# Performance work log

Hardware: AMD Instinct MI355X
Metric: run time of the kernel (lower is better)

The kernel has to match this reference:

```python
import jax, jax.numpy as jnp
import numpy as np

B, T, S_ENC, D = 2, 1024, 1024, 2048
NQ, NKV, H = 16, 8, 256
EPS = 1e-6
CAP = 50.0
SCALE = 0.0625  # query_pre_attn_scalar = head_dim**-0.5
BASE = 10000
K_MASK = -2.3819763e+38


def rms_norm(x, scale, eps=EPS):
    var = jnp.mean(jnp.square(x), axis=-1, keepdims=True)
    return x * jax.lax.rsqrt(var + eps) * (1.0 + scale)


def apply_rope(x, positions, base=BASE):
    # x: [B, L, N, H], positions: [B, L] float. rope_proportion=1.0 -> full head.
    head_dim = x.shape[-1]
    timescale = base ** (2.0 / head_dim * jnp.arange(head_dim // 2, dtype=jnp.float32))
    sinusoid = positions[..., None] / timescale  # [B, L, H/2]
    sinusoid = sinusoid[..., None, :]            # [B, L, 1, H/2]
    sin, cos = jnp.sin(sinusoid), jnp.cos(sinusoid)
    x1, x2 = jnp.split(x, 2, axis=-1)
    return jnp.concatenate([x1 * cos - x2 * sin, x2 * cos + x1 * sin], axis=-1).astype(x.dtype)


def setup_inputs() -> dict:
    key = jax.random.key(0)
    ks = jax.random.split(key, 6)
    hidden_states = jax.random.normal(ks[0], (B, T, D), jnp.float32)
    encoder_hidden_states = jax.random.normal(ks[1], (B, S_ENC, D), jnp.float32)
    position_ids = jnp.broadcast_to(jnp.arange(T, dtype=jnp.int32), (B, T))
    causal = jnp.tril(jnp.ones((T, T), bool))
    merged = jnp.concatenate([causal, jnp.ones((T, S_ENC), bool)], axis=-1)
    merged_attention_mask = jnp.broadcast_to(merged[None, None], (B, 1, T, T + S_ENC))
    q_w = jax.random.normal(ks[2], (NQ, D, H), jnp.float32) * 0.02
    k_w = jax.random.normal(ks[3], (NKV, D, H), jnp.float32) * 0.02
    v_w = jax.random.normal(ks[4], (NKV, D, H), jnp.float32) * 0.02
    o_w = jax.random.normal(ks[5], (NQ, H, D), jnp.float32) * 0.02
    q_scale = jnp.zeros((H,), jnp.float32)
    k_scale = jnp.zeros((H,), jnp.float32)
    return {
        'hidden_states': hidden_states,
        'encoder_hidden_states': encoder_hidden_states,
        'position_ids': position_ids,
        'merged_attention_mask': merged_attention_mask,
        'q_w': q_w, 'k_w': k_w, 'v_w': v_w, 'o_w': o_w,
        'q_scale': q_scale, 'k_scale': k_scale,
    }


def reference(hidden_states, encoder_hidden_states, position_ids, merged_attention_mask,
              q_w, k_w, v_w, o_w, q_scale, k_scale):
    # Fused QKV projections
    q = jnp.einsum('BTD,NDH->BTNH', hidden_states, q_w)
    self_k = jnp.einsum('BTD,NDH->BTNH', hidden_states, k_w)
    self_v = jnp.einsum('BTD,NDH->BTNH', hidden_states, v_w)
    # QK RMSNorm
    q = rms_norm(q, q_scale)
    self_k = rms_norm(self_k, k_scale)
    # RoPE on decoder-side q/k only
    pos = position_ids.astype(jnp.float32)
    q = apply_rope(q, pos)
    self_k = apply_rope(self_k, pos)
    # Cross KV (no RoPE, k-norm applied)
    cross_k = rms_norm(jnp.einsum('BTD,NDH->BTNH', encoder_hidden_states, k_w), k_scale)
    cross_v = jnp.einsum('BTD,NDH->BTNH', encoder_hidden_states, v_w)
    # Merge KV: [B, T+S_enc, NKV, H]
    k = jnp.concatenate([self_k, cross_k], axis=1)
    v = jnp.concatenate([self_v, cross_v], axis=1)
    q = q * SCALE
    # GQA: group query heads over kv heads
    G = NQ // NKV
    qg = q.reshape(B, T, NKV, G, H)
    logits = jnp.einsum('BTKGH,BSKH->BKGTS', qg, k)
    # Logit soft-cap
    logits = CAP * jnp.tanh(logits / CAP)
    mask = merged_attention_mask[:, 0][:, None, None]  # [B,1,1,T,S_comb]
    logits = jnp.where(mask, logits, K_MASK)
    probs = jax.nn.softmax(logits, axis=-1)
    out = jnp.einsum('BKGTS,BSKH->BTKGH', probs, v).reshape(B, T, NQ, H)
    return jnp.einsum('BTNH,NHD->BTD', out, o_w)
```

## Files before the change

### kernel.cpp

```cpp
#include <hip/hip_runtime.h>
#include <hip/hip_bf16.h>
#include <stdint.h>

typedef __hip_bfloat16 bf16;
typedef __attribute__((ext_vector_type(8))) short bv8;
typedef __attribute__((ext_vector_type(4))) float f32x4;


__device__ __forceinline__ f32x4 mfma16(bv8 a, bv8 b, f32x4 c) {
  return __builtin_amdgcn_mfma_f32_16x16x32_bf16(a, b, c, 0, 0, 0);
}

__device__ __forceinline__ void gload16(const void* g, void* lds) {
  __builtin_amdgcn_global_load_lds((const __attribute__((address_space(1))) void*)g,
                                   (__attribute__((address_space(3))) void*)lds, 16, 0, 0);
}

__device__ __forceinline__ void storeC(float* p, float v) { *p = v; }
__device__ __forceinline__ void storeC(bf16* p, float v) { *p = __float2bfloat16(v); }

__global__ void cast_f32_bf16(const float* __restrict__ src, bf16* __restrict__ dst, int n4) {
  int i = blockIdx.x * blockDim.x + threadIdx.x;
  if (i >= n4) return;
  float4 v = reinterpret_cast<const float4*>(src)[i];
  bf16 t[4] = {__float2bfloat16(v.x), __float2bfloat16(v.y),
               __float2bfloat16(v.z), __float2bfloat16(v.w)};
  reinterpret_cast<uint64_t*>(dst)[i] = *reinterpret_cast<uint64_t*>(t);
}

__global__ void transpose_cast(const float* __restrict__ src, bf16* __restrict__ dst,
                               int R, int C) {
  __shared__ float tile[32][33];
  const int z = blockIdx.z;
  const float* s = src + (size_t)z * R * C;
  bf16* d = dst + (size_t)z * R * C;
  const int c0 = blockIdx.x * 32, r0 = blockIdx.y * 32;
  const int x = threadIdx.x, y = threadIdx.y;
#pragma unroll
  for (int i = 0; i < 32; i += 8)
    tile[y + i][x] = s[(size_t)(r0 + y + i) * C + c0 + x];
  __syncthreads();
#pragma unroll
  for (int i = 0; i < 32; i += 8)
    d[(size_t)(c0 + y + i) * R + r0 + x] = __float2bfloat16(tile[x][y + i]);
}

__global__ void transpose_v(const bf16* __restrict__ src, int src_ld,
                            bf16* __restrict__ dst, int t0) {
  __shared__ bf16 tile[32][33];
  const int z = blockIdx.z, b = z >> 3, kvh = z & 7;
  const bf16* s = src + (size_t)(b * 1024) * src_ld + kvh * 256;
  bf16* d = dst + (size_t)(z * 256) * 2048 + t0;
  const int h0 = blockIdx.x * 32, tt0 = blockIdx.y * 32;
  const int x = threadIdx.x, y = threadIdx.y;
#pragma unroll
  for (int i = 0; i < 32; i += 8)
    tile[y + i][x] = s[(size_t)(tt0 + y + i) * src_ld + h0 + x];
  __syncthreads();
#pragma unroll
  for (int i = 0; i < 32; i += 8)
    d[(size_t)(h0 + y + i) * 2048 + tt0 + x] = tile[x][y + i];
}

template <typename CT>
__launch_bounds__(256)
__global__ void gemm_bt(const bf16* __restrict__ A, const bf16* __restrict__ Bt,
                        CT* __restrict__ C, int N, int K) {
  __shared__ __align__(16) bf16 As[128 * 32];
  __shared__ __align__(16) bf16 Bs[128 * 32];
  const int tid = threadIdx.x;
  const int w = tid >> 6, l = tid & 63;
  const int wr = w >> 1, wc = w & 1;
  const int l15 = l & 15, lhi = l >> 4;
  const int m0 = blockIdx.y * 128, n0 = blockIdx.x * 128;
  const bf16* ag = A + (size_t)(m0 + (tid >> 2)) * K + (tid & 3) * 8;
  const bf16* bg = Bt + (size_t)(n0 + (tid >> 2)) * K + (tid & 3) * 8;
  bf16* asw = As + w * 512;
  bf16* bsw = Bs + w * 512;
  f32x4 acc[4][4] = {};
  for (int k0 = 0; k0 < K; k0 += 32) {
    gload16(ag + k0, asw);
    gload16(ag + (size_t)64 * K + k0, asw + 2048);
    gload16(bg + k0, bsw);
    gload16(bg + (size_t)64 * K + k0, bsw + 2048);
    asm volatile("s_waitcnt vmcnt(0)" ::: "memory");
    __syncthreads();
    bv8 af[4], bfv[4];
#pragma unroll
    for (int m = 0; m < 4; ++m)
      af[m] = *reinterpret_cast<const bv8*>(As + (wr * 64 + m * 16 + l15) * 32 + lhi * 8);
#pragma unroll
    for (int n = 0; n < 4; ++n)
      bfv[n] = *reinterpret_cast<const bv8*>(Bs + (wc * 64 + n * 16 + l15) * 32 + lhi * 8);
#pragma unroll
    for (int m = 0; m < 4; ++m)
#pragma unroll
      for (int n = 0; n < 4; ++n)
        acc[m][n] = mfma16(af[m], bfv[n], acc[m][n]);
    __syncthreads();
  }
  const int r0 = m0 + wr * 64 + lhi * 4;
  const int c0 = n0 + wc * 64 + l15;
#pragma unroll
  for (int m = 0; m < 4; ++m)
#pragma unroll
    for (int n = 0; n < 4; ++n) {
      f32x4 v = acc[m][n];
#pragma unroll
      for (int j = 0; j < 4; ++j)
        storeC(&C[(size_t)(r0 + m * 16 + j) * N + c0 + n * 16], v[j]);
    }
}

template <bool ROPE>
__launch_bounds__(256)
__global__ void norm_finalize(const bf16* __restrict__ src, int src_ld, int src_col0,
                              const float* __restrict__ scale,
                              const int* __restrict__ pos_ids,
                              bf16* __restrict__ dst, int nheads, int dst_S, int dst_t0,
                              float mul) {
  const int gid = blockIdx.x * 4 + (threadIdx.x >> 6);
  const int l = threadIdx.x & 63;
  const int token = gid / nheads;
  const int n = gid - token * nheads;
  const int b = token >> 10;
  const int t = token & 1023;
  const size_t soff = (size_t)token * src_ld + src_col0 + n * 256 + l * 4;
  bf16 xb[4];
  *reinterpret_cast<uint64_t*>(xb) = *reinterpret_cast<const uint64_t*>(src + soff);
  float x[4];
#pragma unroll
  for (int c = 0; c < 4; ++c) x[c] = __bfloat162float(xb[c]);
  float ss = x[0] * x[0] + x[1] * x[1] + x[2] * x[2] + x[3] * x[3];
#pragma unroll
  for (int d = 1; d < 64; d <<= 1) ss += __shfl_xor(ss, d);
  const float r = rsqrtf(ss * (1.0f / 256.0f) + 1e-6f);
  float v[4];
#pragma unroll
  for (int c = 0; c < 4; ++c) v[c] = x[c] * r * (1.0f + scale[l * 4 + c]);
  if (ROPE) {
    const float pos = (float)pos_ids[token];
    float o[4];
#pragma unroll
    for (int c = 0; c < 4; ++c) {
      const int j = (l & 31) * 4 + c;
      const float inv_ts = exp2f(-(float)j * 0.10381025296523007f);
      const float arg = pos * inv_ts;
      const float sj = sinf(arg), cj = cosf(arg);
      const float partner = __shfl_xor(v[c], 32);
      o[c] = (l < 32) ? (v[c] * cj - partner * sj) : (v[c] * cj + partner * sj);
    }
#pragma unroll
    for (int c = 0; c < 4; ++c) v[c] = o[c];
  }
  bf16 ob[4];
#pragma unroll
  for (int c = 0; c < 4; ++c) ob[c] = __float2bfloat16(v[c] * mul);
  const size_t doff = ((size_t)((b * nheads + n) * dst_S + dst_t0 + t)) * 256 + l * 4;
  *reinterpret_cast<uint64_t*>(dst + doff) = *reinterpret_cast<uint64_t*>(ob);
}

__launch_bounds__(512, 2)
__global__ void attn_kernel(const bf16* __restrict__ qb, const bf16* __restrict__ kb,
                            const bf16* __restrict__ vt, bf16* __restrict__ attn_out) {
  __shared__ __align__(16) bf16 Ks[2][64 * 256];
  __shared__ __align__(16) bf16 Vs[2][256 * 64];
  __shared__ __align__(16) bf16 pbuf[8][16 * 72];
  const int qt = blockIdx.x;
  const int c  = blockIdx.y;
  const int b = c >> 3, kvh = c & 7;
  const int tid = threadIdx.x, w = tid >> 6, l = tid & 63;
  const int wq = w & 3, g = w >> 2;
  const int n = kvh * 2 + g;
  const int l15 = l & 15, lhi = l >> 4;
  const int xr = (l15 & 7) << 4;

  const bf16* kbase = kb + (size_t)(b * 8 + kvh) * 2048 * 256;
  const bf16* vbase = vt + (size_t)(b * 8 + kvh) * 256 * 2048;

  const bf16* ksrc[4];
  const bf16* vsrc[4];
#pragma unroll
  for (int i = 0; i < 4; ++i) {
    const int r0 = (w * 4 + i) * 2 + (l >> 5);
    const int cbs = ((l & 31) * 16) ^ ((r0 & 7) << 4);
    ksrc[i] = kbase + r0 * 256 + (cbs >> 1);
    const int h0 = (w * 4 + i) * 8 + (l >> 3);
    const int cbv = ((l & 7) * 16) ^ ((h0 & 7) << 4);
    vsrc[i] = vbase + (size_t)h0 * 2048 + (cbv >> 1);
  }

  const bf16* qptr = qb + ((size_t)(b * 16 + n) * 1024 + qt * 64 + wq * 16 + l15) * 256 + lhi * 8;
  bv8 qf[8];
#pragma unroll
  for (int f = 0; f < 8; ++f) qf[f] = *reinterpret_cast<const bv8*>(qptr + f * 32);

  f32x4 oacc[16] = {};
  float rs[4] = {0.f, 0.f, 0.f, 0.f};

  const int nt = qt + 17;

#pragma unroll
  for (int i = 0; i < 4; ++i) gload16(ksrc[i], &Ks[0][(w * 4 + i) * 512]);
#pragma unroll
  for (int i = 0; i < 4; ++i) gload16(vsrc[i], &Vs[0][(w * 4 + i) * 512]);
  asm volatile("s_waitcnt vmcnt(0)" ::: "memory");
  __syncthreads();

  for (int it = 0; it < nt; ++it) {
    const int cur = it & 1;
    if (it + 1 < nt) {
      const int itn = it + 1;
      const int s1 = (itn <= qt) ? itn * 64 : 1024 + (itn - qt - 1) * 64;
#pragma unroll
      for (int i = 0; i < 4; ++i)
        gload16(ksrc[i] + (size_t)s1 * 256, &Ks[cur ^ 1][(w * 4 + i) * 512]);
#pragma unroll
      for (int i = 0; i < 4; ++i)
        gload16(vsrc[i] + s1, &Vs[cur ^ 1][(w * 4 + i) * 512]);
    }
    f32x4 lacc[4] = {};
#pragma unroll
    for (int sub = 0; sub < 4; ++sub) {
      const int rbase = (sub * 16 + l15) * 256;
#pragma unroll
      for (int f = 0; f < 8; ++f) {
        const int off = rbase + (((f * 64 + lhi * 16) ^ xr) >> 1);
        bv8 kf = *reinterpret_cast<const bv8*>(&Ks[cur][off]);
        lacc[sub] = mfma16(qf[f], kf, lacc[sub]);
      }
    }
    const bool diag = (it == qt);
#pragma unroll
    for (int sub = 0; sub < 4; ++sub) {
#pragma unroll
      for (int j = 0; j < 4; ++j) {
        const float raw = lacc[sub][j];
        const float e2 = __expf(raw * 0.04f);
        const bool ok = !diag || (sub * 16 + l15 <= wq * 16 + lhi * 4 + j);
        const float p = ok ? __expf(50.f - __fdividef(100.f, e2 + 1.f)) : 0.f;
        rs[j] += p;
        pbuf[w][(lhi * 4 + j) * 72 + sub * 16 + l15] = __float2bfloat16(p);
      }
    }
    __syncthreads();
#pragma unroll
    for (int ks = 0; ks < 2; ++ks) {
      bv8 pa = *reinterpret_cast<const bv8*>(&pbuf[w][l15 * 72 + ks * 32 + lhi * 8]);
#pragma unroll
      for (int ht = 0; ht < 16; ++ht) {
        const int off = (ht * 16 + l15) * 64 + (((ks * 64 + lhi * 16) ^ xr) >> 1);
        bv8 vf = *reinterpret_cast<const bv8*>(&Vs[cur][off]);
        oacc[ht] = mfma16(pa, vf, oacc[ht]);
      }
    }
    asm volatile("s_waitcnt vmcnt(0)" ::: "memory");
    __syncthreads();
  }
  float invr[4];
#pragma unroll
  for (int j = 0; j < 4; ++j) {
    float s = rs[j];
    s += __shfl_xor(s, 1);
    s += __shfl_xor(s, 2);
    s += __shfl_xor(s, 4);
    s += __shfl_xor(s, 8);
    invr[j] = 1.0f / s;
  }
  bf16* op = attn_out + ((size_t)(b * 1024 + qt * 64 + wq * 16 + lhi * 4) * 4096) + n * 256 + l15;
#pragma unroll
  for (int ht = 0; ht < 16; ++ht)
#pragma unroll
    for (int j = 0; j < 4; ++j)
      op[(size_t)j * 4096 + ht * 16] = __float2bfloat16(oacc[ht][j] * invr[j]);
}

extern "C" void kernel_launch(void* const* d_in, const int* in_sizes, int n_in,
                              void* d_out, int out_size, void* d_ws, size_t ws_size,
                              hipStream_t stream) {
  (void)in_sizes; (void)n_in; (void)out_size; (void)ws_size;
  const float* hidden = (const float*)d_in[0];
  const float* enc    = (const float*)d_in[1];
  const int*   pos    = (const int*)d_in[2];
  const float* q_w = (const float*)d_in[4];
  const float* k_w = (const float*)d_in[5];
  const float* v_w = (const float*)d_in[6];
  const float* o_w = (const float*)d_in[7];
  const float* q_s = (const float*)d_in[8];
  const float* k_s = (const float*)d_in[9];
  float* out = (float*)d_out;

  char* base = (char*)d_ws;
  bf16* hid_b  = (bf16*)(base + 0);
  bf16* enc_b  = (bf16*)(base + 8388608);
  bf16* qb     = (bf16*)(base + 0);
  bf16* wqkvt  = (bf16*)(base + 16777216);
  bf16* kbuf   = (bf16*)(base + 16777216);
  bf16* vtb    = (bf16*)(base + 33554432);
  bf16* owt    = (bf16*)(base + 50331648);
  bf16* cself  = (bf16*)(base + 67108864);
  bf16* attn_b = (bf16*)(base + 67108864);
  bf16* ccross = (bf16*)(base + 100663296);

  dim3 tb32(32, 8);
  cast_f32_bf16<<<4096, 256, 0, stream>>>(hidden, hid_b, 1048576);
  cast_f32_bf16<<<4096, 256, 0, stream>>>(enc, enc_b, 1048576);
  transpose_cast<<<dim3(8, 64, 16), tb32, 0, stream>>>(q_w, wqkvt, 2048, 256);
  transpose_cast<<<dim3(8, 64, 8),  tb32, 0, stream>>>(k_w, wqkvt + 8388608, 2048, 256);
  transpose_cast<<<dim3(8, 64, 8),  tb32, 0, stream>>>(v_w, wqkvt + 12582912, 2048, 256);
  transpose_cast<<<dim3(64, 128, 1), tb32, 0, stream>>>(o_w, owt, 4096, 2048);
  gemm_bt<bf16><<<dim3(64, 16), 256, 0, stream>>>(hid_b, wqkvt, cself, 8192, 2048);
  gemm_bt<bf16><<<dim3(32, 16), 256, 0, stream>>>(enc_b, wqkvt + 8388608, ccross, 4096, 2048);
  norm_finalize<true><<<8192, 256, 0, stream>>>(cself, 8192, 0, q_s, pos, qb, 16, 1024, 0, 0.0625f);
  norm_finalize<true><<<4096, 256, 0, stream>>>(cself, 8192, 4096, k_s, pos, kbuf, 8, 2048, 0, 1.0f);
  norm_finalize<false><<<4096, 256, 0, stream>>>(ccross, 4096, 0, k_s, nullptr, kbuf, 8, 2048, 1024, 1.0f);
  transpose_v<<<dim3(8, 32, 16), tb32, 0, stream>>>(cself + 6144, 8192, vtb, 0);
  transpose_v<<<dim3(8, 32, 16), tb32, 0, stream>>>(ccross + 2048, 4096, vtb, 1024);
  attn_kernel<<<dim3(16, 16), 512, 0, stream>>>(qb, kbuf, vtb, attn_b);
  gemm_bt<float><<<dim3(16, 16), 256, 0, stream>>>(attn_b, owt, out, 2048, 4096);
}
```

Baseline: 453.0 us.

## Process both GQA query heads per wave, reusing K/V fragments, 256-thread blocks

The attention block shrinks from 8 waves (4 query tiles × 2 heads) to 4 waves, and each wave now computes both query heads of its KV group. Every K and V fragment read from LDS feeds two MFMAs, which halves LDS read traffic per MFMA. The block index is also remapped so neighbouring blocks share KV heads, which may help L2 reuse. The cost is twice the accumulator registers (two oacc sets of 16 f32x4), which could lower occupancy or cause spills. Each thread also issues twice as many global-to-LDS loads per stage.

New measurement: 496.1 us. +9.5%, slower.

```diff
diff --git a/kernel.cpp b/kernel.cpp
--- a/kernel.cpp
+++ b/kernel.cpp
@@ -160,50 +160,53 @@
   *reinterpret_cast<uint64_t*>(dst + doff) = *reinterpret_cast<uint64_t*>(ob);
 }
 
-__launch_bounds__(512, 2)
+__launch_bounds__(256, 1)
 __global__ void attn_kernel(const bf16* __restrict__ qb, const bf16* __restrict__ kb,
                             const bf16* __restrict__ vt, bf16* __restrict__ attn_out) {
   __shared__ __align__(16) bf16 Ks[2][64 * 256];
   __shared__ __align__(16) bf16 Vs[2][256 * 64];
-  __shared__ __align__(16) bf16 pbuf[8][16 * 72];
-  const int qt = blockIdx.x;
-  const int c  = blockIdx.y;
-  const int b = c >> 3, kvh = c & 7;
+  __shared__ __align__(16) bf16 pbuf[4][2][16 * 72];
+  const int lin = blockIdx.x + 16 * blockIdx.y;
+  const int kvc = (lin & 7) | (((lin >> 7) & 1) << 3);
+  const int qt  = (lin >> 3) & 15;
+  const int b = kvc >> 3, kvh = kvc & 7;
   const int tid = threadIdx.x, w = tid >> 6, l = tid & 63;
-  const int wq = w & 3, g = w >> 2;
-  const int n = kvh * 2 + g;
   const int l15 = l & 15, lhi = l >> 4;
   const int xr = (l15 & 7) << 4;
 
   const bf16* kbase = kb + (size_t)(b * 8 + kvh) * 2048 * 256;
   const bf16* vbase = vt + (size_t)(b * 8 + kvh) * 256 * 2048;
 
-  const bf16* ksrc[4];
-  const bf16* vsrc[4];
-#pragma unroll
-  for (int i = 0; i < 4; ++i) {
-    const int r0 = (w * 4 + i) * 2 + (l >> 5);
-    const int cbs = ((l & 31) * 16) ^ ((r0 & 7) << 4);
-    ksrc[i] = kbase + r0 * 256 + (cbs >> 1);
-    const int h0 = (w * 4 + i) * 8 + (l >> 3);
-    const int cbv = ((l & 7) * 16) ^ ((h0 & 7) << 4);
-    vsrc[i] = vbase + (size_t)h0 * 2048 + (cbv >> 1);
-  }
-
-  const bf16* qptr = qb + ((size_t)(b * 16 + n) * 1024 + qt * 64 + wq * 16 + l15) * 256 + lhi * 8;
-  bv8 qf[8];
-#pragma unroll
-  for (int f = 0; f < 8; ++f) qf[f] = *reinterpret_cast<const bv8*>(qptr + f * 32);
-
-  f32x4 oacc[16] = {};
-  float rs[4] = {0.f, 0.f, 0.f, 0.f};
+  const int kr = tid >> 5;
+  const int kcb = ((tid & 31) * 16) ^ ((kr & 7) << 4);
+  const bf16* kT = kbase + kr * 256 + (kcb >> 1);
+  const int vr = tid >> 3;
+  const int vcb = ((tid & 7) * 16) ^ ((vr & 7) << 4);
+  const bf16* vT = vbase + (size_t)vr * 2048 + (vcb >> 1);
+
+#define STAGE_KV(bb, s0)                                                        \
+  do {                                                                          \
+    _Pragma("unroll") for (int i = 0; i < 8; ++i)                               \
+        gload16(kT + (size_t)(s0) * 256 + i * 2048, &Ks[bb][i * 2048 + w * 512]); \
+    _Pragma("unroll") for (int i = 0; i < 8; ++i)                               \
+        gload16(vT + (s0) + (size_t)i * 65536, &Vs[bb][i * 2048 + w * 512]);    \
+  } while (0)
+
+  bv8 qf[2][8];
+#pragma unroll
+  for (int g = 0; g < 2; ++g) {
+    const bf16* qp = qb +
+        ((size_t)(b * 16 + kvh * 2 + g) * 1024 + qt * 64 + w * 16 + l15) * 256 + lhi * 8;
+#pragma unroll
+    for (int f = 0; f < 8; ++f) qf[g][f] = *reinterpret_cast<const bv8*>(qp + f * 32);
+  }
+
+  f32x4 oacc[2][16] = {};
+  float rs[2][4] = {};
 
   const int nt = qt + 17;
 
-#pragma unroll
-  for (int i = 0; i < 4; ++i) gload16(ksrc[i], &Ks[0][(w * 4 + i) * 512]);
-#pragma unroll
-  for (int i = 0; i < 4; ++i) gload16(vsrc[i], &Vs[0][(w * 4 + i) * 512]);
+  STAGE_KV(0, 0);
   asm volatile("s_waitcnt vmcnt(0)" ::: "memory");
   __syncthreads();
 
@@ -212,14 +215,9 @@
     if (it + 1 < nt) {
       const int itn = it + 1;
       const int s1 = (itn <= qt) ? itn * 64 : 1024 + (itn - qt - 1) * 64;
-#pragma unroll
-      for (int i = 0; i < 4; ++i)
-        gload16(ksrc[i] + (size_t)s1 * 256, &Ks[cur ^ 1][(w * 4 + i) * 512]);
-#pragma unroll
-      for (int i = 0; i < 4; ++i)
-        gload16(vsrc[i] + s1, &Vs[cur ^ 1][(w * 4 + i) * 512]);
-    }
-    f32x4 lacc[4] = {};
+      STAGE_KV(cur ^ 1, s1);
+    }
+    f32x4 lacc[2][4] = {};
 #pragma unroll
     for (int sub = 0; sub < 4; ++sub) {
       const int rbase = (sub * 16 + l15) * 256;
@@ -227,52 +225,61 @@
       for (int f = 0; f < 8; ++f) {
         const int off = rbase + (((f * 64 + lhi * 16) ^ xr) >> 1);
         bv8 kf = *reinterpret_cast<const bv8*>(&Ks[cur][off]);
-        lacc[sub] = mfma16(qf[f], kf, lacc[sub]);
+        lacc[0][sub] = mfma16(qf[0][f], kf, lacc[0][sub]);
+        lacc[1][sub] = mfma16(qf[1][f], kf, lacc[1][sub]);
       }
     }
     const bool diag = (it == qt);
 #pragma unroll
-    for (int sub = 0; sub < 4; ++sub) {
-#pragma unroll
-      for (int j = 0; j < 4; ++j) {
-        const float raw = lacc[sub][j];
-        const float e2 = __expf(raw * 0.04f);
-        const bool ok = !diag || (sub * 16 + l15 <= wq * 16 + lhi * 4 + j);
-        const float p = ok ? __expf(50.f - __fdividef(100.f, e2 + 1.f)) : 0.f;
-        rs[j] += p;
-        pbuf[w][(lhi * 4 + j) * 72 + sub * 16 + l15] = __float2bfloat16(p);
-      }
-    }
+    for (int g = 0; g < 2; ++g)
+#pragma unroll
+      for (int sub = 0; sub < 4; ++sub)
+#pragma unroll
+        for (int j = 0; j < 4; ++j) {
+          const float raw = lacc[g][sub][j];
+          const float e2 = __expf(raw * 0.04f);
+          const bool ok = !diag || (sub * 16 + l15 <= w * 16 + lhi * 4 + j);
+          const float p = ok ? __expf(50.f - __fdividef(100.f, e2 + 1.f)) : 0.f;
+          rs[g][j] += p;
+          pbuf[w][g][(lhi * 4 + j) * 72 + sub * 16 + l15] = __float2bfloat16(p);
+        }
     __syncthreads();
 #pragma unroll
     for (int ks = 0; ks < 2; ++ks) {
-      bv8 pa = *reinterpret_cast<const bv8*>(&pbuf[w][l15 * 72 + ks * 32 + lhi * 8]);
+      bv8 pa0 = *reinterpret_cast<const bv8*>(&pbuf[w][0][l15 * 72 + ks * 32 + lhi * 8]);
+      bv8 pa1 = *reinterpret_cast<const bv8*>(&pbuf[w][1][l15 * 72 + ks * 32 + lhi * 8]);
 #pragma unroll
       for (int ht = 0; ht < 16; ++ht) {
         const int off = (ht * 16 + l15) * 64 + (((ks * 64 + lhi * 16) ^ xr) >> 1);
         bv8 vf = *reinterpret_cast<const bv8*>(&Vs[cur][off]);
-        oacc[ht] = mfma16(pa, vf, oacc[ht]);
+        oacc[0][ht] = mfma16(pa0, vf, oacc[0][ht]);
+        oacc[1][ht] = mfma16(pa1, vf, oacc[1][ht]);
       }
     }
     asm volatile("s_waitcnt vmcnt(0)" ::: "memory");
     __syncthreads();
   }
-  float invr[4];
-#pragma unroll
-  for (int j = 0; j < 4; ++j) {
-    float s = rs[j];
-    s += __shfl_xor(s, 1);
-    s += __shfl_xor(s, 2);
-    s += __shfl_xor(s, 4);
-    s += __shfl_xor(s, 8);
-    invr[j] = 1.0f / s;
-  }
-  bf16* op = attn_out + ((size_t)(b * 1024 + qt * 64 + wq * 16 + lhi * 4) * 4096) + n * 256 + l15;
-#pragma unroll
-  for (int ht = 0; ht < 16; ++ht)
-#pragma unroll
-    for (int j = 0; j < 4; ++j)
-      op[(size_t)j * 4096 + ht * 16] = __float2bfloat16(oacc[ht][j] * invr[j]);
+#undef STAGE_KV
+#pragma unroll
+  for (int g = 0; g < 2; ++g) {
+    float invr[4];
+#pragma unroll
+    for (int j = 0; j < 4; ++j) {
+      float s = rs[g][j];
+      s += __shfl_xor(s, 1);
+      s += __shfl_xor(s, 2);
+      s += __shfl_xor(s, 4);
+      s += __shfl_xor(s, 8);
+      invr[j] = 1.0f / s;
+    }
+    bf16* op = attn_out + ((size_t)(b * 1024 + qt * 64 + w * 16 + lhi * 4) * 4096) +
+               (kvh * 2 + g) * 256 + l15;
+#pragma unroll
+    for (int ht = 0; ht < 16; ++ht)
+#pragma unroll
+      for (int j = 0; j < 4; ++j)
+        op[(size_t)j * 4096 + ht * 16] = __float2bfloat16(oacc[g][ht][j] * invr[j]);
+  }
 }
 
 extern "C" void kernel_launch(void* const* d_in, const int* in_sizes, int n_in,
@@ -316,6 +323,6 @@
   norm_finalize<false><<<4096, 256, 0, stream>>>(ccross, 4096, 0, k_s, nullptr, kbuf, 8, 2048, 1024, 1.0f);
   transpose_v<<<dim3(8, 32, 16), tb32, 0, stream>>>(cself + 6144, 8192, vtb, 0);
   transpose_v<<<dim3(8, 32, 16), tb32, 0, stream>>>(ccross + 2048, 4096, vtb, 1024);
-  attn_kernel<<<dim3(16, 16), 512, 0, stream>>>(qb, kbuf, vtb, attn_b);
+  attn_kernel<<<dim3(16, 16), 256, 0, stream>>>(qb, kbuf, vtb, attn_b);
   gemm_bt<float><<<dim3(16, 16), 256, 0, stream>>>(attn_b, owt, out, 2048, 4096);
 }
```
